# Performance work log

Measured on AMD Instinct MI355X. Metric: run time of the kernel, lower is better.

## Reference

```python
import jax, jax.numpy as jnp
import numpy as np

KH, KW = 3, 3
STRIDE = (1, 1)


def setup_inputs() -> dict:
    key = jax.random.key(0)
    k1, k2, k3 = jax.random.split(key, 3)
    N, C, H, W = 16, 128, 64, 64
    O = 128
    x = jax.random.normal(k1, (N, C, H, W), dtype=jnp.float32)
    # Flat weight layout [O, C*KH*KW], matching torch reshape of [O,C,KH,KW]
    weight = jax.random.normal(k2, (O, C * KH * KW), dtype=jnp.float32) * 0.02
    bias = jax.random.normal(k3, (O, 1), dtype=jnp.float32) * 0.02
    return {"x": x, "weight": weight, "bias": bias}


def reference(x, weight, bias):
    O = weight.shape[0]
    C = x.shape[1]
    # [O, C*KH*KW] -> [O, C, KH, KW]; flattening order (C major, then kh, kw)
    # matches the module's unfold/permute im2col layout.
    w4 = weight.reshape(O, C, KH, KW)
    out = jax.lax.conv_general_dilated(
        x, w4,
        window_strides=STRIDE,
        padding='VALID',
        dimension_numbers=('NCHW', 'OIHW', 'NCHW'),
    )
    return out + bias.reshape(1, O, 1, 1)
```

## Files before the change

### kernel.cpp

```cpp
#include <hip/hip_runtime.h>
#include <stdint.h>

#define AS_G __attribute__((address_space(1)))
#define AS_L __attribute__((address_space(3)))

typedef __bf16 bf16x8 __attribute__((ext_vector_type(8)));
typedef float  f32x4  __attribute__((ext_vector_type(4)));

static constexpr int NIMG = 16, CIN = 128, H = 64, W = 64, OCH = 128;
static constexpr int HO = 62, WO = 62;
static constexpr int PIX = HO * WO;
static constexpr int M_TOT = NIMG * PIX;
static constexpr int K_TOT = CIN * 9;
static constexpr int BM = 64, BK = 64;
static constexpr int KSTEPS = K_TOT / BK;
static constexpr int BUFB = 24576;

__device__ __forceinline__ unsigned short f2bf(float f) {
    union { float f; uint32_t u; } v; v.f = f;
    uint32_t u = v.u;
    return (unsigned short)((u + 0x7FFFu + ((u >> 16) & 1u)) >> 16);
}

__global__ __launch_bounds__(256) void prep_kernel(const float* __restrict__ x,
                                                   const float* __restrict__ wsrc,
                                                   unsigned short* __restrict__ xt,
                                                   unsigned short* __restrict__ bpd) {
    __shared__ float lds[CIN][W + 4];
    if (blockIdx.x < NIMG * H) {
        const int n   = blockIdx.x >> 6;
        const int h   = blockIdx.x & 63;
        const int tid = threadIdx.x;
        {
            const int c  = tid >> 1;
            const int w0 = (tid & 1) * 32;
            const float* src = x + (((size_t)(n * CIN + c) * H + h) * W + w0);
            #pragma unroll
            for (int j = 0; j < 8; ++j) {
                float4 v = *reinterpret_cast<const float4*>(src + j * 4);
                *reinterpret_cast<float4*>(&lds[c][w0 + j * 4]) = v;
            }
        }
        __syncthreads();
        {
            const int w  = tid >> 2;
            const int c0 = (tid & 3) * 32;
            unsigned short* dst = xt + (((size_t)(n * H + h) * W + w) * CIN + c0);
            uint32_t pk[16];
            #pragma unroll
            for (int j = 0; j < 16; ++j) {
                uint32_t lo = f2bf(lds[c0 + 2 * j][w]);
                uint32_t hi = f2bf(lds[c0 + 2 * j + 1][w]);
                pk[j] = lo | (hi << 16);
            }
            #pragma unroll
            for (int j = 0; j < 4; ++j) {
                *reinterpret_cast<uint4*>(dst + j * 8) =
                    make_uint4(pk[4 * j], pk[4 * j + 1], pk[4 * j + 2], pk[4 * j + 3]);
            }
        }
    } else {
        int tid = (blockIdx.x - NIMG * H) * 256 + threadIdx.x;
        if (tid < OCH * K_TOT) {
            int o  = tid / K_TOT;
            int kp = tid - o * K_TOT;
            int t  = kp >> 7;
            int c  = kp & 127;
            bpd[tid] = f2bf(wsrc[o * K_TOT + c * 9 + t]);
        }
    }
}

__global__ __launch_bounds__(256) void gemm_kernel(const unsigned short* __restrict__ xt,
                                                   const unsigned short* __restrict__ bp,
                                                   const float* __restrict__ bias,
                                                   float* __restrict__ out) {
    __shared__ alignas(16) char lds[2 * BUFB];
    const int tid  = threadIdx.x;
    const int wv   = tid >> 6;
    const int lane = tid & 63;
    const int m0   = blockIdx.x * BM;

    const int csel = ((lane & 7) ^ (lane >> 3)) * 8;
    int aBase[2], bBase[4];
    #pragma unroll
    for (int i = 0; i < 2; ++i) {
        int row = (wv * 2 + i) * 8 + (lane >> 3);
        int m = m0 + row;
        int n  = m / PIX;
        int r  = m - n * PIX;
        int y  = r / WO;
        int xx = r - y * WO;
        aBase[i] = ((n * H + y) * W + xx) * CIN;
    }
    #pragma unroll
    for (int i = 0; i < 4; ++i)
        bBase[i] = ((wv * 4 + i) * 8 + (lane >> 3)) * K_TOT;

    auto stage = [&](int buf, int step) {
        const int t  = step >> 1;
        const int c0 = (step & 1) * 64;
        const int tapoff = (t / 3) * (W * CIN) + (t % 3) * CIN + c0;
        const int kb = step * BK;
        char* dst = lds + buf * BUFB;
        #pragma unroll
        for (int i = 0; i < 2; ++i)
            __builtin_amdgcn_global_load_lds(
                (AS_G unsigned int*)(xt + aBase[i] + tapoff + csel),
                (AS_L unsigned int*)(dst + (wv * 2 + i) * 1024), 16, 0, 0);
        #pragma unroll
        for (int i = 0; i < 4; ++i)
            __builtin_amdgcn_global_load_lds(
                (AS_G unsigned int*)(bp + bBase[i] + kb + csel),
                (AS_L unsigned int*)(dst + 8192 + (wv * 4 + i) * 1024), 16, 0, 0);
    };

    const int wr = wv >> 1, wc = wv & 1;
    const int lr = lane & 15, lq = lane >> 4;
    const int aRow = (wr * 32 + lr) * 128;
    const int bRow = (wc * 64 + lr) * 128;
    int colx[2];
    #pragma unroll
    for (int ks = 0; ks < 2; ++ks)
        colx[ks] = (ks * 64 + lq * 16) ^ ((lane & 7) << 4);

    f32x4 acc[2][4];
    #pragma unroll
    for (int a = 0; a < 2; ++a)
        #pragma unroll
        for (int b = 0; b < 4; ++b)
            acc[a][b] = (f32x4){0.f, 0.f, 0.f, 0.f};

    stage(0, 0);
    __syncthreads();

    #pragma unroll 2
    for (int step = 0; step < KSTEPS; ++step) {
        const int buf = step & 1;
        if (step + 1 < KSTEPS) stage(buf ^ 1, step + 1);
        const char* base = lds + buf * BUFB;
        #pragma unroll
        for (int ks = 0; ks < 2; ++ks) {
            bf16x8 af[2], bfr[4];
            #pragma unroll
            for (int mi = 0; mi < 2; ++mi)
                af[mi] = *(const bf16x8*)(base + aRow + mi * 2048 + colx[ks]);
            #pragma unroll
            for (int ni = 0; ni < 4; ++ni)
                bfr[ni] = *(const bf16x8*)(base + 8192 + bRow + ni * 2048 + colx[ks]);
            #pragma unroll
            for (int mi = 0; mi < 2; ++mi)
                #pragma unroll
                for (int ni = 0; ni < 4; ++ni)
                    acc[mi][ni] = __builtin_amdgcn_mfma_f32_16x16x32_bf16(
                        bfr[ni], af[mi], acc[mi][ni], 0, 0, 0);
        }
        __syncthreads();
    }

    f32x4 bv[4];
    #pragma unroll
    for (int ni = 0; ni < 4; ++ni)
        bv[ni] = *(const f32x4*)(bias + wc * 64 + ni * 16 + lq * 4);
    #pragma unroll
    for (int mi = 0; mi < 2; ++mi) {
        int m = m0 + wr * 32 + mi * 16 + lr;
        int n  = m / PIX;
        int r  = m - n * PIX;
        int y  = r / WO;
        int xx = r - y * WO;
        float* ob = out + (size_t)n * OCH * PIX + y * WO + xx;
        #pragma unroll
        for (int ni = 0; ni < 4; ++ni)
            #pragma unroll
            for (int j = 0; j < 4; ++j) {
                int o = wc * 64 + ni * 16 + lq * 4 + j;
                ob[(size_t)o * PIX] = acc[mi][ni][j] + bv[ni][j];
            }
    }
}

extern "C" void kernel_launch(void* const* d_in, const int* in_sizes, int n_in,
                              void* d_out, int out_size, void* d_ws, size_t ws_size,
                              hipStream_t stream) {
    const float* x    = (const float*)d_in[0];
    const float* wsrc = (const float*)d_in[1];
    const float* bias = (const float*)d_in[2];
    float* out = (float*)d_out;
    unsigned short* xt = (unsigned short*)d_ws;
    unsigned short* bp = xt + (size_t)NIMG * H * W * CIN;
    prep_kernel<<<dim3(NIMG * H + (OCH * K_TOT + 255) / 256), dim3(256), 0, stream>>>(
        x, wsrc, xt, bp);
    gemm_kernel<<<dim3(M_TOT / BM), dim3(256), 0, stream>>>(xt, bp, bias, out);
}
```

Measured before the change: 48.72 us.

## Restructure conv GEMM: 128-row tiles, direct global A loads, full-channel weight staging

The implicit-GEMM kernel changes to BM=128 output pixels per block. Each wave owns 32 rows across all 128 output channels, so the 2x2 warp split is gone. Activation fragments are now read straight from global memory into registers instead of being staged through LDS. Only the weights are double-buffered in LDS, one full 3x3 tap (128 channels by 128 outputs) per iteration, which cuts barriers from 18 to 9. In exchange there are more accumulator registers, uncoalesced per-lane global A loads that depend on cache hits, and a tail block with bounds guards.

```diff
diff --git a/kernel.cpp b/kernel.cpp
--- a/kernel.cpp
+++ b/kernel.cpp
@@ -12,9 +12,9 @@
 static constexpr int PIX = HO * WO;
 static constexpr int M_TOT = NIMG * PIX;
 static constexpr int K_TOT = CIN * 9;
-static constexpr int BM = 64, BK = 64;
-static constexpr int KSTEPS = K_TOT / BK;
-static constexpr int BUFB = 24576;
+static constexpr int BM = 128;
+static constexpr int NCHUNK = 9;
+static constexpr int GRID = (M_TOT + BM - 1) / BM;
 
 __device__ __forceinline__ unsigned short f2bf(float f) {
     union { float f; uint32_t u; } v; v.f = f;
@@ -75,108 +75,93 @@
                                                    const unsigned short* __restrict__ bp,
                                                    const float* __restrict__ bias,
                                                    float* __restrict__ out) {
-    __shared__ alignas(16) char lds[2 * BUFB];
+    __shared__ alignas(16) char lds[2 * 32768];
     const int tid  = threadIdx.x;
     const int wv   = tid >> 6;
     const int lane = tid & 63;
+    const int lr   = lane & 15, lq = lane >> 4;
     const int m0   = blockIdx.x * BM;
 
-    const int csel = ((lane & 7) ^ (lane >> 3)) * 8;
-    int aBase[2], bBase[4];
+    int bOff[8];
     #pragma unroll
-    for (int i = 0; i < 2; ++i) {
-        int row = (wv * 2 + i) * 8 + (lane >> 3);
-        int m = m0 + row;
+    for (int p = 0; p < 8; ++p) {
+        int s = (wv * 8 + p) * 64 + lane;
+        int o = s >> 4, q = s & 15;
+        bOff[p] = o * K_TOT + ((q ^ (o & 7)) * 8);
+    }
+    auto stageB = [&](int buf, int t) {
+        const unsigned short* src = bp + t * 128;
+        char* dst = lds + buf * 32768;
+        #pragma unroll
+        for (int p = 0; p < 8; ++p)
+            __builtin_amdgcn_global_load_lds(
+                (AS_G unsigned int*)(src + bOff[p]),
+                (AS_L unsigned int*)(dst + (wv * 8 + p) * 1024), 16, 0, 0);
+    };
+
+    int base0[2], ybase[2];
+    bool valid[2];
+    #pragma unroll
+    for (int mi = 0; mi < 2; ++mi) {
+        int m = m0 + wv * 32 + mi * 16 + lr;
+        valid[mi] = (m < M_TOT);
+        if (m >= M_TOT) m = M_TOT - 1;
         int n  = m / PIX;
         int r  = m - n * PIX;
         int y  = r / WO;
         int xx = r - y * WO;
-        aBase[i] = ((n * H + y) * W + xx) * CIN;
+        base0[mi] = ((n * H + y) * W + xx) * CIN + lq * 8;
+        ybase[mi] = n * OCH * PIX + y * WO + xx;
     }
-    #pragma unroll
-    for (int i = 0; i < 4; ++i)
-        bBase[i] = ((wv * 4 + i) * 8 + (lane >> 3)) * K_TOT;
 
-    auto stage = [&](int buf, int step) {
-        const int t  = step >> 1;
-        const int c0 = (step & 1) * 64;
-        const int tapoff = (t / 3) * (W * CIN) + (t % 3) * CIN + c0;
-        const int kb = step * BK;
-        char* dst = lds + buf * BUFB;
-        #pragma unroll
-        for (int i = 0; i < 2; ++i)
-            __builtin_amdgcn_global_load_lds(
-                (AS_G unsigned int*)(xt + aBase[i] + tapoff + csel),
-                (AS_L unsigned int*)(dst + (wv * 2 + i) * 1024), 16, 0, 0);
-        #pragma unroll
-        for (int i = 0; i < 4; ++i)
-            __builtin_amdgcn_global_load_lds(
-                (AS_G unsigned int*)(bp + bBase[i] + kb + csel),
-                (AS_L unsigned int*)(dst + 8192 + (wv * 4 + i) * 1024), 16, 0, 0);
-    };
-
-    const int wr = wv >> 1, wc = wv & 1;
-    const int lr = lane & 15, lq = lane >> 4;
-    const int aRow = (wr * 32 + lr) * 128;
-    const int bRow = (wc * 64 + lr) * 128;
-    int colx[2];
-    #pragma unroll
-    for (int ks = 0; ks < 2; ++ks)
-        colx[ks] = (ks * 64 + lq * 16) ^ ((lane & 7) << 4);
-
-    f32x4 acc[2][4];
+    f32x4 acc[2][8];
     #pragma unroll
     for (int a = 0; a < 2; ++a)
         #pragma unroll
-        for (int b = 0; b < 4; ++b)
+        for (int b = 0; b < 8; ++b)
             acc[a][b] = (f32x4){0.f, 0.f, 0.f, 0.f};
 
-    stage(0, 0);
+    stageB(0, 0);
     __syncthreads();
 
-    #pragma unroll 2
-    for (int step = 0; step < KSTEPS; ++step) {
-        const int buf = step & 1;
-        if (step + 1 < KSTEPS) stage(buf ^ 1, step + 1);
-        const char* base = lds + buf * BUFB;
+    const int wxor = (lr & 7) << 4;
+    for (int t = 0; t < NCHUNK; ++t) {
+        if (t + 1 < NCHUNK) stageB((t & 1) ^ 1, t + 1);
+        const char* wb = lds + (t & 1) * 32768;
+        const int kh = t / 3, kw = t - kh * 3;
+        const int tapoff = (kh * W + kw) * CIN;
         #pragma unroll
-        for (int ks = 0; ks < 2; ++ks) {
-            bf16x8 af[2], bfr[4];
+        for (int ks = 0; ks < 4; ++ks) {
+            bf16x8 af[2], wf[8];
             #pragma unroll
             for (int mi = 0; mi < 2; ++mi)
-                af[mi] = *(const bf16x8*)(base + aRow + mi * 2048 + colx[ks]);
+                af[mi] = *(const bf16x8*)(xt + base0[mi] + tapoff + ks * 32);
+            const int colw = (ks * 64 + lq * 16) ^ wxor;
             #pragma unroll
-            for (int ni = 0; ni < 4; ++ni)
-                bfr[ni] = *(const bf16x8*)(base + 8192 + bRow + ni * 2048 + colx[ks]);
+            for (int ni = 0; ni < 8; ++ni)
+                wf[ni] = *(const bf16x8*)(wb + ni * 4096 + lr * 256 + colw);
             #pragma unroll
             for (int mi = 0; mi < 2; ++mi)
                 #pragma unroll
-                for (int ni = 0; ni < 4; ++ni)
+                for (int ni = 0; ni < 8; ++ni)
                     acc[mi][ni] = __builtin_amdgcn_mfma_f32_16x16x32_bf16(
-                        bfr[ni], af[mi], acc[mi][ni], 0, 0, 0);
+                        wf[ni], af[mi], acc[mi][ni], 0, 0, 0);
         }
         __syncthreads();
     }
 
-    f32x4 bv[4];
-    #pragma unroll
-    for (int ni = 0; ni < 4; ++ni)
-        bv[ni] = *(const f32x4*)(bias + wc * 64 + ni * 16 + lq * 4);
     #pragma unroll
     for (int mi = 0; mi < 2; ++mi) {
-        int m = m0 + wr * 32 + mi * 16 + lr;
-        int n  = m / PIX;
-        int r  = m - n * PIX;
-        int y  = r / WO;
-        int xx = r - y * WO;
-        float* ob = out + (size_t)n * OCH * PIX + y * WO + xx;
-        #pragma unroll
-        for (int ni = 0; ni < 4; ++ni)
+        if (valid[mi]) {
+            float* ob = out + ybase[mi];
             #pragma unroll
-            for (int j = 0; j < 4; ++j) {
-                int o = wc * 64 + ni * 16 + lq * 4 + j;
-                ob[(size_t)o * PIX] = acc[mi][ni][j] + bv[ni][j];
+            for (int ni = 0; ni < 8; ++ni) {
+                f32x4 bv = *(const f32x4*)(bias + ni * 16 + lq * 4);
+                #pragma unroll
+                for (int j = 0; j < 4; ++j)
+                    ob[(size_t)(ni * 16 + lq * 4 + j) * PIX] = acc[mi][ni][j] + bv[j];
             }
+        }
     }
 }
 
@@ -191,5 +176,5 @@
     unsigned short* bp = xt + (size_t)NIMG * H * W * CIN;
     prep_kernel<<<dim3(NIMG * H + (OCH * K_TOT + 255) / 256), dim3(256), 0, stream>>>(
         x, wsrc, xt, bp);
-    gemm_kernel<<<dim3(M_TOT / BM), dim3(256), 0, stream>>>(xt, bp, bias, out);
+    gemm_kernel<<<dim3(GRID), dim3(256), 0, stream>>>(xt, bp, bias, out);
 }
```

Result: faster. 47.36 us (-2.8%).
